# Kernel optimization log

Hardware: AMD Instinct MI355X
Metric: run time of the kernel (lower is better)

The kernel has to match this reference:

```python
import jax, jax.numpy as jnp
import numpy as np

D_MODEL = 1024
H = 16
D = D_MODEL // H  # 64 per-head dim
B, T = 2, 2048


def setup_inputs() -> dict:
    key = jax.random.key(0)
    ks = jax.random.split(key, 5)
    scale = 1.0 / np.sqrt(D_MODEL)
    x = jax.random.normal(ks[0], (B, T, D_MODEL), dtype=jnp.float32)
    Wqkv = jax.random.normal(ks[1], (D_MODEL, 3 * D_MODEL), dtype=jnp.float32) * scale
    bqkv = jnp.zeros((3 * D_MODEL,), dtype=jnp.float32)
    Wproj = jax.random.normal(ks[2], (D_MODEL, D_MODEL), dtype=jnp.float32) * scale
    bproj = jnp.zeros((D_MODEL,), dtype=jnp.float32)
    return {"x": x, "Wqkv": Wqkv, "bqkv": bqkv, "Wproj": Wproj, "bproj": bproj}


def reference(x, Wqkv, bqkv, Wproj, bproj):
    b, t, d_model = x.shape
    h, d = H, D
    qkv = x @ Wqkv + bqkv  # [b, t, 3*d_model]
    q, k, v = jnp.split(qkv, 3, axis=-1)
    # [b, t, d_model] -> [b, h, t, d]
    q = q.reshape(b, t, h, d).transpose(0, 2, 1, 3)
    k = k.reshape(b, t, h, d).transpose(0, 2, 1, 3)
    v = v.reshape(b, t, h, d).transpose(0, 2, 1, 3)
    att = jnp.einsum('bhqd,bhkd->bhqk', q, k) / jnp.sqrt(jnp.float32(d))
    causal = jnp.tril(jnp.ones((t, t), dtype=bool))  # [t, t]
    att = jnp.where(causal[None, None, :, :], att, -jnp.inf)
    att = jax.nn.softmax(att, axis=-1)
    # dropout in eval mode -> identity (deterministic reference)
    out = jnp.einsum('bhqk,bhkd->bhqd', att, v)  # [b, h, t, d]
    out = out.transpose(0, 2, 1, 3).reshape(b, t, d_model)
    out = out @ Wproj + bproj
    return out
```

## Files before the change

kernel.cpp:

```cpp
#include <hip/hip_runtime.h>
#include <cstddef>

typedef __bf16 bf16x8 __attribute__((ext_vector_type(8)));
typedef float  f32x4  __attribute__((ext_vector_type(4)));

__device__ __forceinline__ float bf2f(unsigned short s) {
    return __uint_as_float(((unsigned int)s) << 16);
}
__device__ __forceinline__ unsigned short f2bf(float x) {
    unsigned int u = __float_as_uint(x);
    unsigned int r = u + 0x7fffu + ((u >> 16) & 1u);
    return (unsigned short)(r >> 16);
}

__device__ __forceinline__ void async_load16(const void* g, void* l) {
    __builtin_amdgcn_global_load_lds(
        (const __attribute__((address_space(1))) unsigned int*)g,
        (__attribute__((address_space(3))) unsigned int*)l,
        16, 0, 0);
}

__global__ __launch_bounds__(256) void detect_dtype_kernel(
    const unsigned short* __restrict__ x, int* __restrict__ flag)
{
    __shared__ int cnt;
    if (threadIdx.x == 0) cnt = 0;
    __syncthreads();
    int wild = 0;
    for (int k = 0; k < 16; ++k) {
        unsigned short u = x[(size_t)((k * 256 + threadIdx.x) << 1)];
        int e = (u >> 7) & 0xFF;
        wild += ((e >= 0x90) || (e >= 1 && e <= 0x48)) ? 1 : 0;
    }
    atomicAdd(&cnt, wild);
    __syncthreads();
    if (threadIdx.x == 0) *flag = (cnt > 512) ? 1 : 0;
}

__global__ __launch_bounds__(256) void cast_kernel(
    const int* __restrict__ flag, const void* __restrict__ src,
    unsigned short* __restrict__ dst, int n8)
{
    const int i = blockIdx.x * 256 + threadIdx.x;
    if (i >= n8) return;
    const size_t off = (size_t)i * 8;
    if (*flag) {
        const float* s = (const float*)src + off;
        float4 a = *(const float4*)s;
        float4 b = *(const float4*)(s + 4);
        uint4 o;
        o.x = (unsigned)f2bf(a.x) | ((unsigned)f2bf(a.y) << 16);
        o.y = (unsigned)f2bf(a.z) | ((unsigned)f2bf(a.w) << 16);
        o.z = (unsigned)f2bf(b.x) | ((unsigned)f2bf(b.y) << 16);
        o.w = (unsigned)f2bf(b.z) | ((unsigned)f2bf(b.w) << 16);
        *(uint4*)(dst + off) = o;
    } else {
        *(uint4*)(dst + off) = *(const uint4*)((const unsigned short*)src + off);
    }
}

__global__ __launch_bounds__(256) void transpose_cast_kernel(
    const int* __restrict__ flag, const void* __restrict__ src,
    unsigned short* __restrict__ dst, int R, int C)
{
    __shared__ unsigned short T[64][72];
    const int c0 = blockIdx.x * 64, r0 = blockIdx.y * 64;
    const int t  = threadIdx.x;
    const int r  = t >> 2, cl = (t & 3) << 4;

    unsigned short v[16];
    if (*flag) {
        const float* s = (const float*)src + (size_t)(r0 + r) * C + c0 + cl;
        #pragma unroll
        for (int q = 0; q < 4; ++q) {
            float4 a = *(const float4*)(s + q * 4);
            v[q * 4 + 0] = f2bf(a.x); v[q * 4 + 1] = f2bf(a.y);
            v[q * 4 + 2] = f2bf(a.z); v[q * 4 + 3] = f2bf(a.w);
        }
    } else {
        const unsigned short* s = (const unsigned short*)src + (size_t)(r0 + r) * C + c0 + cl;
        uint4 a = *(const uint4*)s;
        uint4 b = *(const uint4*)(s + 8);
        unsigned int w[8] = {a.x, a.y, a.z, a.w, b.x, b.y, b.z, b.w};
        #pragma unroll
        for (int q = 0; q < 8; ++q) {
            v[q * 2]     = (unsigned short)(w[q] & 0xffffu);
            v[q * 2 + 1] = (unsigned short)(w[q] >> 16);
        }
    }
    #pragma unroll
    for (int c = 0; c < 16; ++c) T[cl + c][r] = v[c];
    __syncthreads();

    const int c = t >> 2, rl = (t & 3) << 4;
    uint4 o0 = *(const uint4*)&T[c][rl];
    uint4 o1 = *(const uint4*)&T[c][rl + 8];
    unsigned short* dp = dst + (size_t)(c0 + c) * R + r0 + rl;
    *(uint4*)dp       = o0;
    *(uint4*)(dp + 8) = o1;
}

__device__ __forceinline__ void bt_mainloop(
    const unsigned short* __restrict__ A,
    const unsigned short* __restrict__ BT,
    int K, int m0, int n0,
    unsigned short* As, unsigned short* Bs,
    f32x4 (&acc)[4][4])
{
    const int tid  = threadIdx.x;
    const int wave = tid >> 6;
    const int lane = tid & 63;
    const int mrow = lane & 15;
    const int quad = lane >> 4;
    const int wr = wave >> 1, wc = wave & 1;
    const int srow = tid >> 2;
    const int scol = (tid & 3) << 3;

    const unsigned short* ga  = A  + (size_t)(m0 + srow) * K + scol;
    const unsigned short* ga2 = ga + (size_t)64 * K;
    const unsigned short* gb  = BT + (size_t)(n0 + srow) * K + scol;
    const unsigned short* gb2 = gb + (size_t)64 * K;
    unsigned short* lA  = As + wave * 512;
    unsigned short* lA2 = As + 2048 + wave * 512;
    unsigned short* lB  = Bs + wave * 512;
    unsigned short* lB2 = Bs + 2048 + wave * 512;

    for (int k0 = 0; k0 < K; k0 += 32) {
        async_load16(ga,  lA);
        async_load16(ga2, lA2);
        async_load16(gb,  lB);
        async_load16(gb2, lB2);
        ga += 32; ga2 += 32; gb += 32; gb2 += 32;
        __syncthreads();

        bf16x8 afr[4], bfr[4];
        #pragma unroll
        for (int mt = 0; mt < 4; ++mt)
            afr[mt] = *(const bf16x8*)(As + (wr * 64 + mt * 16 + mrow) * 32 + quad * 8);
        #pragma unroll
        for (int nt = 0; nt < 4; ++nt)
            bfr[nt] = *(const bf16x8*)(Bs + (wc * 64 + nt * 16 + mrow) * 32 + quad * 8);
        #pragma unroll
        for (int mt = 0; mt < 4; ++mt) {
            #pragma unroll
            for (int nt = 0; nt < 4; ++nt)
                acc[mt][nt] = __builtin_amdgcn_mfma_f32_16x16x32_bf16(
                    afr[mt], bfr[nt], acc[mt][nt], 0, 0, 0);
        }
        __syncthreads();
    }
}

__global__ __launch_bounds__(256) void gemm_qkv_bt(
    const int* __restrict__ flag,
    const unsigned short* __restrict__ A,
    const unsigned short* __restrict__ BT,
    const void* __restrict__ bias,
    unsigned short* __restrict__ Qb, unsigned short* __restrict__ Kb,
    unsigned short* __restrict__ VbT)
{
    __shared__ unsigned short As[128 * 32];
    __shared__ unsigned short Bs[128 * 32];
    const int m0 = blockIdx.y * 128, n0 = blockIdx.x * 128;

    f32x4 acc[4][4];
    #pragma unroll
    for (int mt = 0; mt < 4; ++mt)
        #pragma unroll
        for (int nt = 0; nt < 4; ++nt)
            { acc[mt][nt][0]=0.f; acc[mt][nt][1]=0.f; acc[mt][nt][2]=0.f; acc[mt][nt][3]=0.f; }

    bt_mainloop(A, BT, 1024, m0, n0, As, Bs, acc);

    const int tid  = threadIdx.x;
    const int wave = tid >> 6;
    const int lane = tid & 63;
    const int mrow = lane & 15;
    const int quad = lane >> 4;
    const int wr = wave >> 1, wc = wave & 1;
    const bool f32b = (*flag != 0);

    #pragma unroll
    for (int nt = 0; nt < 4; ++nt) {
        const int n = n0 + wc * 64 + nt * 16 + mrow;
        const float bv = f32b ? ((const float*)bias)[n]
                              : bf2f(((const unsigned short*)bias)[n]);
        const int sel = n >> 10;
        const int h   = (n & 1023) >> 6;
        const int d   = n & 63;
        const float sc = (sel == 0) ? 0.125f : 1.0f;
        #pragma unroll
        for (int mt = 0; mt < 4; ++mt) {
            #pragma unroll
            for (int r = 0; r < 4; ++r) {
                const int m  = m0 + wr * 64 + mt * 16 + quad * 4 + r;
                const int bb = m >> 11;
                const int t  = m & 2047;
                const unsigned short ov = f2bf((acc[mt][nt][r] + bv) * sc);
                const int bhh = bb * 16 + h;
                if (sel == 0)      Qb [(((size_t)bhh * 2048 + t) << 6) + d] = ov;
                else if (sel == 1) Kb [(((size_t)bhh * 2048 + t) << 6) + d] = ov;
                else               VbT[((((size_t)bhh << 6) + d) << 11) + t] = ov;
            }
        }
    }
}

__global__ __launch_bounds__(256) void gemm_proj_bt(
    const int* __restrict__ flag,
    const unsigned short* __restrict__ A,
    const unsigned short* __restrict__ BT,
    const void* __restrict__ bias, void* __restrict__ Out)
{
    __shared__ unsigned short As[128 * 32];
    __shared__ unsigned short Bs[128 * 32];
    const int m0 = blockIdx.y * 128, n0 = blockIdx.x * 128;

    f32x4 acc[4][4];
    #pragma unroll
    for (int mt = 0; mt < 4; ++mt)
        #pragma unroll
        for (int nt = 0; nt < 4; ++nt)
            { acc[mt][nt][0]=0.f; acc[mt][nt][1]=0.f; acc[mt][nt][2]=0.f; acc[mt][nt][3]=0.f; }

    bt_mainloop(A, BT, 1024, m0, n0, As, Bs, acc);

    const int tid  = threadIdx.x;
    const int wave = tid >> 6;
    const int lane = tid & 63;
    const int mrow = lane & 15;
    const int quad = lane >> 4;
    const int wr = wave >> 1, wc = wave & 1;
    const bool f32b = (*flag != 0);

    #pragma unroll
    for (int nt = 0; nt < 4; ++nt) {
        const int n = n0 + wc * 64 + nt * 16 + mrow;
        const float bv = f32b ? ((const float*)bias)[n]
                              : bf2f(((const unsigned short*)bias)[n]);
        #pragma unroll
        for (int mt = 0; mt < 4; ++mt) {
            #pragma unroll
            for (int r = 0; r < 4; ++r) {
                const int m = m0 + wr * 64 + mt * 16 + quad * 4 + r;
                const float val = acc[mt][nt][r] + bv;
                if (f32b) ((float*)Out)[(size_t)m * 1024 + n] = val;
                else      ((unsigned short*)Out)[(size_t)m * 1024 + n] = f2bf(val);
            }
        }
    }
}

__global__ __launch_bounds__(256) void attn_kernel(
    const unsigned short* __restrict__ Qb,
    const unsigned short* __restrict__ Kb,
    const unsigned short* __restrict__ VbT,
    unsigned short* __restrict__ Attn)
{
    __shared__ unsigned short KsH[2][128 * 32];
    __shared__ unsigned short VsQ[4][64 * 32];
    __shared__ unsigned short Ps[64][136];

    const int tid  = threadIdx.x;
    const int wave = tid >> 6;
    const int lane = tid & 63;
    const int mrow = lane & 15;
    const int quad = lane >> 4;

    const int blk   = blockIdx.x;
    const int xcd   = blk & 7;
    const int slot  = blk >> 3;
    const int bh    = (xcd << 2) | (slot & 3);
    const int qpair = slot >> 2;
    const int b     = bh >> 4, h = bh & 15;

    const int krow  = tid >> 2;
    const int kcol8 = (tid & 3) << 3;

    const unsigned short* Qbase = Qb  + ((size_t)bh << 17);
    const unsigned short* Kbase = Kb  + ((size_t)bh << 17);
    const unsigned short* Vtb   = VbT + ((size_t)bh << 17);

    bf16x8 ones;
    #pragma unroll
    for (int e = 0; e < 8; ++e) ones[e] = (__bf16)1.0f;

    for (int half = 0; half < 2; ++half) {
        const int qblk = (half == 0) ? qpair : (31 - qpair);
        const int q0   = qblk << 6;
        const int nr   = (qblk >> 1) + 1;

        bf16x8 aq[2];
        {
            const unsigned short* qp = Qbase + (size_t)(q0 + wave * 16 + mrow) * 64 + quad * 8;
            aq[0] = *(const bf16x8*)qp;
            aq[1] = *(const bf16x8*)(qp + 32);
        }

        f32x4 Oa[4];
        #pragma unroll
        for (int dt = 0; dt < 4; ++dt) { Oa[dt][0]=0.f; Oa[dt][1]=0.f; Oa[dt][2]=0.f; Oa[dt][3]=0.f; }
        float m_run[4] = {-1e30f, -1e30f, -1e30f, -1e30f};
        float l_run[4] = {0.f, 0.f, 0.f, 0.f};

        for (int rr = 0; rr < nr; ++rr) {
            const int kt0 = rr << 7;

            #pragma unroll
            for (int h2 = 0; h2 < 2; ++h2) {
                #pragma unroll
                for (int p = 0; p < 2; ++p) {
                    const unsigned short* src =
                        Kbase + (size_t)(kt0 + p * 64 + krow) * 64 + h2 * 32 + kcol8;
                    async_load16(src, &KsH[h2][(p * 64 + krow) * 32 + kcol8]);
                }
            }
            #pragma unroll
            for (int q4 = 0; q4 < 4; ++q4) {
                const unsigned short* src =
                    Vtb + ((size_t)krow << 11) + kt0 + q4 * 32 + kcol8;
                async_load16(src, &VsQ[q4][krow * 32 + kcol8]);
            }
            __syncthreads();

            f32x4 sacc[8];
            #pragma unroll
            for (int jt = 0; jt < 8; ++jt) { sacc[jt][0]=0.f; sacc[jt][1]=0.f; sacc[jt][2]=0.f; sacc[jt][3]=0.f; }
            #pragma unroll
            for (int ks = 0; ks < 2; ++ks) {
                #pragma unroll
                for (int jt = 0; jt < 8; ++jt) {
                    bf16x8 bk = *(const bf16x8*)&KsH[ks][(jt * 16 + mrow) * 32 + quad * 8];
                    sacc[jt] = __builtin_amdgcn_mfma_f32_16x16x32_bf16(aq[ks], bk, sacc[jt], 0, 0, 0);
                }
            }

            if (rr == nr - 1) {
                #pragma unroll
                for (int jt = 0; jt < 8; ++jt) {
                    const int jg = kt0 + jt * 16 + mrow;
                    #pragma unroll
                    for (int r = 0; r < 4; ++r) {
                        if (jg > q0 + wave * 16 + quad * 4 + r) sacc[jt][r] = -1e30f;
                    }
                }
            }

            float mx[4], alpha[4];
            #pragma unroll
            for (int r = 0; r < 4; ++r) {
                mx[r] = fmaxf(fmaxf(fmaxf(sacc[0][r], sacc[1][r]), fmaxf(sacc[2][r], sacc[3][r])),
                              fmaxf(fmaxf(sacc[4][r], sacc[5][r]), fmaxf(sacc[6][r], sacc[7][r])));
            }
            #pragma unroll
            for (int m = 1; m <= 8; m <<= 1) {
                #pragma unroll
                for (int r = 0; r < 4; ++r) mx[r] = fmaxf(mx[r], __shfl_xor(mx[r], m));
            }
            #pragma unroll
            for (int r = 0; r < 4; ++r) {
                const float m_new = fmaxf(m_run[r], mx[r]);
                alpha[r] = __expf(m_run[r] - m_new);
                m_run[r] = m_new;
            }

            #pragma unroll
            for (int jt = 0; jt < 8; ++jt) {
                #pragma unroll
                for (int r = 0; r < 4; ++r) {
                    const float pv = __expf(sacc[jt][r] - m_run[r]);
                    Ps[wave * 16 + quad * 4 + r][jt * 16 + mrow] = f2bf(pv);
                }
            }

            #pragma unroll
            for (int dt = 0; dt < 4; ++dt) {
                #pragma unroll
                for (int r = 0; r < 4; ++r) Oa[dt][r] *= alpha[r];
            }

            __threadfence_block();

            f32x4 lt; lt[0]=0.f; lt[1]=0.f; lt[2]=0.f; lt[3]=0.f;
            #pragma unroll
            for (int ks4 = 0; ks4 < 4; ++ks4) {
                bf16x8 ap = *(const bf16x8*)&Ps[wave * 16 + mrow][ks4 * 32 + quad * 8];
                lt = __builtin_amdgcn_mfma_f32_16x16x32_bf16(ap, ones, lt, 0, 0, 0);
                #pragma unroll
                for (int dt = 0; dt < 4; ++dt) {
                    bf16x8 bv = *(const bf16x8*)&VsQ[ks4][(dt * 16 + mrow) * 32 + quad * 8];
                    Oa[dt] = __builtin_amdgcn_mfma_f32_16x16x32_bf16(ap, bv, Oa[dt], 0, 0, 0);
                }
            }
            #pragma unroll
            for (int r = 0; r < 4; ++r) l_run[r] = l_run[r] * alpha[r] + lt[r];

            __syncthreads();
        }

        #pragma unroll
        for (int r = 0; r < 4; ++r) {
            const float inv = 1.0f / l_run[r];
            const int t = q0 + wave * 16 + quad * 4 + r;
            const size_t base = ((size_t)(b * 2048 + t)) * 1024 + h * 64;
            #pragma unroll
            for (int dt = 0; dt < 4; ++dt)
                Attn[base + dt * 16 + mrow] = f2bf(Oa[dt][r] * inv);
        }
    }
}

extern "C" void kernel_launch(void* const* d_in, const int* in_sizes, int n_in,
                              void* d_out, int out_size, void* d_ws, size_t ws_size,
                              hipStream_t stream)
{
    const void* x     = d_in[0];
    const void* Wqkv  = d_in[1];
    const void* bqkv  = d_in[2];
    const void* Wproj = d_in[3];
    const void* bproj = d_in[4];

    int* flag = (int*)d_ws;
    unsigned short* ws = (unsigned short*)d_ws;
    unsigned short* xb     = ws + 64;
    unsigned short* shared = xb + 4194304;
    unsigned short* WqkvT  = shared;
    unsigned short* Attn   = shared;
    unsigned short* WprojT = shared + 4194304;
    unsigned short* Qb     = WprojT + 1048576;
    unsigned short* Kb     = Qb + 4194304;
    unsigned short* VbT    = Kb + 4194304;

    detect_dtype_kernel<<<1, 256, 0, stream>>>((const unsigned short*)x, flag);
    cast_kernel<<<2048, 256, 0, stream>>>(flag, x, xb, 524288);
    transpose_cast_kernel<<<dim3(48, 16), 256, 0, stream>>>(flag, Wqkv, WqkvT, 1024, 3072);
    transpose_cast_kernel<<<dim3(16, 16), 256, 0, stream>>>(flag, Wproj, WprojT, 1024, 1024);
    gemm_qkv_bt<<<dim3(24, 32), 256, 0, stream>>>(flag, xb, WqkvT, bqkv, Qb, Kb, VbT);
    attn_kernel<<<512, 256, 0, stream>>>(Qb, Kb, VbT, Attn);
    gemm_proj_bt<<<dim3(8, 32), 256, 0, stream>>>(flag, Attn, WprojT, bproj, d_out);
}
```

Before: 214.5 us.

## Double-buffer K/V tiles with 64-key blocks in attention kernel

```diff
diff --git a/kernel.cpp b/kernel.cpp
--- a/kernel.cpp
+++ b/kernel.cpp
@@ -257,9 +257,9 @@
     const unsigned short* __restrict__ VbT,
     unsigned short* __restrict__ Attn)
 {
-    __shared__ unsigned short KsH[2][128 * 32];
-    __shared__ unsigned short VsQ[4][64 * 32];
-    __shared__ unsigned short Ps[64][136];
+    __shared__ unsigned short Ks2[2][2][64 * 32];
+    __shared__ unsigned short Vs2[2][2][64 * 32];
+    __shared__ unsigned short Ps[64][72];
 
     const int tid  = threadIdx.x;
     const int wave = tid >> 6;
@@ -288,7 +288,7 @@
     for (int half = 0; half < 2; ++half) {
         const int qblk = (half == 0) ? qpair : (31 - qpair);
         const int q0   = qblk << 6;
-        const int nr   = (qblk >> 1) + 1;
+        const int nr   = qblk + 1;
 
         bf16x8 aq[2];
         {
@@ -303,41 +303,52 @@
         float m_run[4] = {-1e30f, -1e30f, -1e30f, -1e30f};
         float l_run[4] = {0.f, 0.f, 0.f, 0.f};
 
+        __syncthreads();
+        {
+            #pragma unroll
+            for (int h2 = 0; h2 < 2; ++h2)
+                async_load16(Kbase + (size_t)krow * 64 + h2 * 32 + kcol8,
+                             &Ks2[0][h2][krow * 32 + kcol8]);
+            #pragma unroll
+            for (int j2 = 0; j2 < 2; ++j2)
+                async_load16(Vtb + ((size_t)krow << 11) + j2 * 32 + kcol8,
+                             &Vs2[0][j2][krow * 32 + kcol8]);
+        }
+
         for (int rr = 0; rr < nr; ++rr) {
-            const int kt0 = rr << 7;
-
-            #pragma unroll
-            for (int h2 = 0; h2 < 2; ++h2) {
-                #pragma unroll
-                for (int p = 0; p < 2; ++p) {
-                    const unsigned short* src =
-                        Kbase + (size_t)(kt0 + p * 64 + krow) * 64 + h2 * 32 + kcol8;
-                    async_load16(src, &KsH[h2][(p * 64 + krow) * 32 + kcol8]);
-                }
-            }
-            #pragma unroll
-            for (int q4 = 0; q4 < 4; ++q4) {
-                const unsigned short* src =
-                    Vtb + ((size_t)krow << 11) + kt0 + q4 * 32 + kcol8;
-                async_load16(src, &VsQ[q4][krow * 32 + kcol8]);
-            }
             __syncthreads();
 
-            f32x4 sacc[8];
-            #pragma unroll
-            for (int jt = 0; jt < 8; ++jt) { sacc[jt][0]=0.f; sacc[jt][1]=0.f; sacc[jt][2]=0.f; sacc[jt][3]=0.f; }
+            if (rr + 1 < nr) {
+                const int nt0 = (rr + 1) << 6;
+                const int nb  = (rr + 1) & 1;
+                #pragma unroll
+                for (int h2 = 0; h2 < 2; ++h2)
+                    async_load16(Kbase + (size_t)(nt0 + krow) * 64 + h2 * 32 + kcol8,
+                                 &Ks2[nb][h2][krow * 32 + kcol8]);
+                #pragma unroll
+                for (int j2 = 0; j2 < 2; ++j2)
+                    async_load16(Vtb + ((size_t)krow << 11) + nt0 + j2 * 32 + kcol8,
+                                 &Vs2[nb][j2][krow * 32 + kcol8]);
+            }
+
+            const int cb  = rr & 1;
+            const int kt0 = rr << 6;
+
+            f32x4 sacc[4];
+            #pragma unroll
+            for (int jt = 0; jt < 4; ++jt) { sacc[jt][0]=0.f; sacc[jt][1]=0.f; sacc[jt][2]=0.f; sacc[jt][3]=0.f; }
             #pragma unroll
             for (int ks = 0; ks < 2; ++ks) {
                 #pragma unroll
-                for (int jt = 0; jt < 8; ++jt) {
-                    bf16x8 bk = *(const bf16x8*)&KsH[ks][(jt * 16 + mrow) * 32 + quad * 8];
+                for (int jt = 0; jt < 4; ++jt) {
+                    bf16x8 bk = *(const bf16x8*)&Ks2[cb][ks][(jt * 16 + mrow) * 32 + quad * 8];
                     sacc[jt] = __builtin_amdgcn_mfma_f32_16x16x32_bf16(aq[ks], bk, sacc[jt], 0, 0, 0);
                 }
             }
 
             if (rr == nr - 1) {
                 #pragma unroll
-                for (int jt = 0; jt < 8; ++jt) {
+                for (int jt = 0; jt < 4; ++jt) {
                     const int jg = kt0 + jt * 16 + mrow;
                     #pragma unroll
                     for (int r = 0; r < 4; ++r) {
@@ -348,10 +359,8 @@
 
             float mx[4], alpha[4];
             #pragma unroll
-            for (int r = 0; r < 4; ++r) {
-                mx[r] = fmaxf(fmaxf(fmaxf(sacc[0][r], sacc[1][r]), fmaxf(sacc[2][r], sacc[3][r])),
-                              fmaxf(fmaxf(sacc[4][r], sacc[5][r]), fmaxf(sacc[6][r], sacc[7][r])));
-            }
+            for (int r = 0; r < 4; ++r)
+                mx[r] = fmaxf(fmaxf(sacc[0][r], sacc[1][r]), fmaxf(sacc[2][r], sacc[3][r]));
             #pragma unroll
             for (int m = 1; m <= 8; m <<= 1) {
                 #pragma unroll
@@ -365,7 +374,7 @@
             }
 
             #pragma unroll
-            for (int jt = 0; jt < 8; ++jt) {
+            for (int jt = 0; jt < 4; ++jt) {
                 #pragma unroll
                 for (int r = 0; r < 4; ++r) {
                     const float pv = __expf(sacc[jt][r] - m_run[r]);
@@ -383,19 +392,17 @@
 
             f32x4 lt; lt[0]=0.f; lt[1]=0.f; lt[2]=0.f; lt[3]=0.f;
             #pragma unroll
-            for (int ks4 = 0; ks4 < 4; ++ks4) {
-                bf16x8 ap = *(const bf16x8*)&Ps[wave * 16 + mrow][ks4 * 32 + quad * 8];
+            for (int ks2 = 0; ks2 < 2; ++ks2) {
+                bf16x8 ap = *(const bf16x8*)&Ps[wave * 16 + mrow][ks2 * 32 + quad * 8];
                 lt = __builtin_amdgcn_mfma_f32_16x16x32_bf16(ap, ones, lt, 0, 0, 0);
                 #pragma unroll
                 for (int dt = 0; dt < 4; ++dt) {
-                    bf16x8 bv = *(const bf16x8*)&VsQ[ks4][(dt * 16 + mrow) * 32 + quad * 8];
+                    bf16x8 bv = *(const bf16x8*)&Vs2[cb][ks2][(dt * 16 + mrow) * 32 + quad * 8];
                     Oa[dt] = __builtin_amdgcn_mfma_f32_16x16x32_bf16(ap, bv, Oa[dt], 0, 0, 0);
                 }
             }
             #pragma unroll
             for (int r = 0; r < 4; ++r) l_run[r] = l_run[r] * alpha[r] + lt[r];
-
-            __syncthreads();
         }
 
         #pragma unroll
```

Measured after the change: 212.4 us. About the same (-1.0%).
